# Kernel optimization log

Measured on AMD Instinct MI355X. Metric: run time of the kernel, lower is better.

The kernel has to match this reference:

```python
import jax, jax.numpy as jnp
import numpy as np

DIM = 768        # channel dim C
HEADS = 12       # num_heads
MAXLEN = 128     # max_seq_len == window length N
NW = 64          # num_windows
B = 4            # batch


def setup_inputs() -> dict:
    key = jax.random.key(0)
    k0, k1, k2, k3 = jax.random.split(key, 4)
    B_ = NW * B
    x = jax.random.normal(k0, (B_, MAXLEN, DIM), jnp.float32)
    mask = jnp.zeros((NW, MAXLEN, MAXLEN), jnp.float32)  # 0/-inf additive window mask
    qkv_w = jax.random.normal(k1, (3 * DIM, DIM), jnp.float32) * 0.02
    bias_table = jax.random.normal(k2, (2 * MAXLEN - 1, HEADS), jnp.float32) * 0.02
    proj_w = jax.random.normal(k3, (DIM, DIM), jnp.float32) * 0.02
    proj_b = jnp.zeros((DIM,), jnp.float32)
    return {"x": x, "mask": mask, "qkv_w": qkv_w, "bias_table": bias_table,
            "proj_w": proj_w, "proj_b": proj_b}


def reference(x, mask, qkv_w, bias_table, proj_w, proj_b):
    B_, N, C = x.shape
    H = HEADS
    hd = C // H
    scale = hd ** -0.5
    # qkv projection (no bias): (B_, N, 3, H, hd)
    qkv = (x @ qkv_w.T).reshape(B_, N, 3, H, hd)
    q = qkv[:, :, 0].transpose(0, 2, 1, 3) * scale  # (B_, H, N, hd)
    k = qkv[:, :, 1].transpose(0, 2, 1, 3)
    v = qkv[:, :, 2].transpose(0, 2, 1, 3)
    attn = jnp.einsum('bhnd,bhmd->bhnm', q, k)       # (B_, H, N, N)
    # relative position bias gather
    coords = jnp.arange(N)
    rel_idx = coords[:, None] - coords[None, :] + (MAXLEN - 1)  # (N, N)
    bias = bias_table[rel_idx]                        # (N, N, H)
    attn = attn + bias.transpose(2, 0, 1)[None]       # (B_, H, N, N)
    # window mask add (mask ndim == 3 branch)
    nW = mask.shape[0]
    attn = attn.reshape(B_ // nW, nW, H, N, N) + mask[None, :, None]
    attn = jax.nn.softmax(attn.reshape(B_, H, N, N), axis=-1)
    out = jnp.einsum('bhnm,bhmd->bhnd', attn, v)      # (B_, H, N, hd)
    out = out.transpose(0, 2, 1, 3).reshape(B_, N, C)
    return out @ proj_w.T + proj_b
```

## Files before the change

kernel.cpp:

```cpp
#include <hip/hip_runtime.h>
#include <hip/hip_bf16.h>
#include <stdint.h>

typedef unsigned short u16;
typedef __bf16 bf16x8 __attribute__((ext_vector_type(8)));
typedef float f32x4 __attribute__((ext_vector_type(4)));

__device__ __forceinline__ u16 f2bf(float f) {
  union { float f; uint32_t u; } v; v.f = f;
  uint32_t u = v.u;
  return (u16)((u + 0x7FFFu + ((u >> 16) & 1u)) >> 16);
}

__device__ __forceinline__ f32x4 mfma16(bf16x8 a, bf16x8 b, f32x4 c) {
  return __builtin_amdgcn_mfma_f32_16x16x32_bf16(a, b, c, 0, 0, 0);
}

#define GLOBAL_TO_LDS16(g, l)                                                  \
  __builtin_amdgcn_global_load_lds(                                            \
      (const __attribute__((address_space(1))) void*)(g),                      \
      (__attribute__((address_space(3))) void*)(l), 16, 0, 0)

__global__ void cvt_bf16_all(const float* __restrict__ x, u16* __restrict__ xb,
                             const float* __restrict__ qw, u16* __restrict__ qwb,
                             const float* __restrict__ pw, u16* __restrict__ pwb) {
  int blk = blockIdx.x;
  const float* src; u16* dst; int i;
  if (blk < 24576)        { src = x;  dst = xb;  i = blk * 256 + threadIdx.x; }
  else if (blk < 26304)   { src = qw; dst = qwb; i = (blk - 24576) * 256 + threadIdx.x; }
  else                    { src = pw; dst = pwb; i = (blk - 26304) * 256 + threadIdx.x; }
  float4 f = ((const float4*)src)[i];
  ushort4 o;
  o.x = f2bf(f.x); o.y = f2bf(f.y); o.z = f2bf(f.z); o.w = f2bf(f.w);
  ((ushort4*)dst)[i] = o;
}

template <bool SWAP>
__global__ __launch_bounds__(256) void qkv_gemm(
    const u16* __restrict__ A, const u16* __restrict__ Bt, int nbase,
    u16* __restrict__ q, u16* __restrict__ k, u16* __restrict__ vT) {
  const int K = 768;
  __shared__ u16 As[128 * 64];
  __shared__ u16 Bs[128 * 64];
  int tid = threadIdx.x;
  int wave = tid >> 6, lane = tid & 63;
  int quad = lane >> 4, lrow = lane & 15;
  int m0 = blockIdx.y * 128, n0 = nbase + blockIdx.x * 128;
  int wr = (wave >> 1) * 64, wc = (wave & 1) * 64;

  const u16* asrc[4]; const u16* bsrc[4]; int ldst[4];
#pragma unroll
  for (int s = 0; s < 4; s++) {
    int p = (wave * 4 + s) * 64 + lane;
    int row = p >> 3, cp = p & 7;
    int c = cp ^ (row & 7);
    asrc[s] = A + (size_t)(m0 + row) * K + c * 8;
    bsrc[s] = Bt + (size_t)(n0 + row) * K + c * 8;
    ldst[s] = p * 8;
  }
  f32x4 acc[4][4] = {};
  for (int k0 = 0; k0 < K; k0 += 64) {
#pragma unroll
    for (int s = 0; s < 4; s++) {
      GLOBAL_TO_LDS16(asrc[s] + k0, As + ldst[s]);
      GLOBAL_TO_LDS16(bsrc[s] + k0, Bs + ldst[s]);
    }
    __syncthreads();
#pragma unroll
    for (int kk = 0; kk < 2; kk++) {
      bf16x8 am[4], bn[4];
#pragma unroll
      for (int i = 0; i < 4; i++) {
        int r = wr + i * 16 + lrow;
        am[i] = *(const bf16x8*)(As + r * 64 + ((((kk << 2) | quad) ^ (r & 7)) << 3));
      }
#pragma unroll
      for (int j = 0; j < 4; j++) {
        int r = wc + j * 16 + lrow;
        bn[j] = *(const bf16x8*)(Bs + r * 64 + ((((kk << 2) | quad) ^ (r & 7)) << 3));
      }
#pragma unroll
      for (int i = 0; i < 4; i++)
#pragma unroll
        for (int j = 0; j < 4; j++)
          acc[i][j] = SWAP ? mfma16(bn[i], am[j], acc[i][j])
                           : mfma16(am[i], bn[j], acc[i][j]);
    }
    __syncthreads();
  }
  int b = m0 >> 7;
  if (SWAP) {
    int t = n0 / 768;
    float s = (t == 0) ? 0.125f : 1.0f;
    u16* dst = (t == 0) ? q : k;
#pragma unroll
    for (int i = 0; i < 4; i++) {
      int nb = (n0 - t * 768) + wc + i * 16 + quad * 4;
      int h = nb >> 6, d0 = nb & 63;
#pragma unroll
      for (int j = 0; j < 4; j++) {
        int seq = wr + j * 16 + lrow;
        ushort4 o;
        o.x = f2bf(acc[i][j][0] * s); o.y = f2bf(acc[i][j][1] * s);
        o.z = f2bf(acc[i][j][2] * s); o.w = f2bf(acc[i][j][3] * s);
        *(ushort4*)(dst + ((size_t)(b * 12 + h)) * 8192 + seq * 64 + d0) = o;
      }
    }
  } else {
#pragma unroll
    for (int j = 0; j < 4; j++) {
      int nb = (n0 - 1536) + wc + j * 16 + lrow;
      int h = nb >> 6, d = nb & 63;
#pragma unroll
      for (int i = 0; i < 4; i++) {
        int seq0 = wr + i * 16 + quad * 4;
        ushort4 o;
        o.x = f2bf(acc[i][j][0]); o.y = f2bf(acc[i][j][1]);
        o.z = f2bf(acc[i][j][2]); o.w = f2bf(acc[i][j][3]);
        *(ushort4*)(vT + ((size_t)(b * 12 + h)) * 8192 + d * 128 + seq0) = o;
      }
    }
  }
}

__global__ __launch_bounds__(512) void attn_kernel(
    const u16* __restrict__ q, const u16* __restrict__ k, const u16* __restrict__ vT,
    const float* __restrict__ mask, const float* __restrict__ bias_table,
    u16* __restrict__ attn_out) {
  __shared__ u16 smem[2 * 128 * 64];
  __shared__ u16 vTs[64 * 128];
  __shared__ float bias_s[255];
  u16* qs = smem;
  u16* ks = smem + 128 * 64;
  u16* ps = smem;
  int tid = threadIdx.x;
  int wave = tid >> 6, lane = tid & 63;
  int quad = lane >> 4, lrow = lane & 15;
  int bh = blockIdx.x;
  int b = bh / 12, h = bh - b * 12;
  int w = b & 63;
  if (tid < 255) bias_s[tid] = bias_table[tid * 12 + h];
  const u16* qg = q + (size_t)bh * 8192;
  const u16* kg = k + (size_t)bh * 8192;
  const u16* vg = vT + (size_t)bh * 8192;
#pragma unroll
  for (int s = 0; s < 2; s++) {
    int p = s * 512 + tid;
    int row = p >> 3, c = (p & 7) ^ (row & 7);
    GLOBAL_TO_LDS16(qg + row * 64 + c * 8, qs + p * 8);
    GLOBAL_TO_LDS16(kg + row * 64 + c * 8, ks + p * 8);
    int dd = p >> 4, cv = (p & 15) ^ (dd & 7);
    GLOBAL_TO_LDS16(vg + dd * 128 + cv * 8, vTs + p * 8);
  }
  __syncthreads();

  int row = wave * 16 + lrow;
  f32x4 sacc[8] = {};
#pragma unroll
  for (int kk = 0; kk < 2; kk++) {
    bf16x8 qf = *(const bf16x8*)(qs + row * 64 + ((((kk << 2) | quad) ^ (row & 7)) << 3));
#pragma unroll
    for (int i = 0; i < 8; i++) {
      int rk = i * 16 + lrow;
      bf16x8 kf = *(const bf16x8*)(ks + rk * 64 + ((((kk << 2) | quad) ^ (rk & 7)) << 3));
      sacc[i] = mfma16(kf, qf, sacc[i]);
    }
  }
  const float* mrow = mask + (size_t)w * 16384 + row * 128;
#pragma unroll
  for (int i = 0; i < 8; i++) {
    int c0 = i * 16 + quad * 4;
    float4 m4 = *(const float4*)(mrow + c0);
    sacc[i][0] += bias_s[row - (c0 + 0) + 127] + m4.x;
    sacc[i][1] += bias_s[row - (c0 + 1) + 127] + m4.y;
    sacc[i][2] += bias_s[row - (c0 + 2) + 127] + m4.z;
    sacc[i][3] += bias_s[row - (c0 + 3) + 127] + m4.w;
  }
  float mx = sacc[0][0];
#pragma unroll
  for (int i = 0; i < 8; i++)
#pragma unroll
    for (int r = 0; r < 4; r++) mx = fmaxf(mx, sacc[i][r]);
  mx = fmaxf(mx, __shfl_xor(mx, 16, 64));
  mx = fmaxf(mx, __shfl_xor(mx, 32, 64));
  float sum = 0.f;
#pragma unroll
  for (int i = 0; i < 8; i++)
#pragma unroll
    for (int r = 0; r < 4; r++) {
      float e = __expf(sacc[i][r] - mx);
      sacc[i][r] = e;
      sum += e;
    }
  sum += __shfl_xor(sum, 16, 64);
  sum += __shfl_xor(sum, 32, 64);
  float inv = 1.f / sum;
  __syncthreads();
#pragma unroll
  for (int i = 0; i < 8; i++) {
    int chunk = i * 2 + (quad >> 1);
    int pos = chunk ^ (row & 7);
    ushort4 o;
    o.x = f2bf(sacc[i][0] * inv); o.y = f2bf(sacc[i][1] * inv);
    o.z = f2bf(sacc[i][2] * inv); o.w = f2bf(sacc[i][3] * inv);
    *(ushort4*)(ps + row * 128 + pos * 8 + (quad & 1) * 4) = o;
  }
  __syncthreads();

  f32x4 oacc[4] = {};
#pragma unroll
  for (int kk = 0; kk < 4; kk++) {
    bf16x8 pf = *(const bf16x8*)(ps + row * 128 + ((((kk << 2) | quad) ^ (row & 7)) << 3));
#pragma unroll
    for (int jd = 0; jd < 4; jd++) {
      int rd = jd * 16 + lrow;
      bf16x8 vf = *(const bf16x8*)(vTs + rd * 128 + ((((kk << 2) | quad) ^ (rd & 7)) << 3));
      oacc[jd] = mfma16(vf, pf, oacc[jd]);
    }
  }
#pragma unroll
  for (int jd = 0; jd < 4; jd++) {
    int d0 = jd * 16 + quad * 4;
    int seq = wave * 16 + lrow;
    ushort4 o;
    o.x = f2bf(oacc[jd][0]); o.y = f2bf(oacc[jd][1]);
    o.z = f2bf(oacc[jd][2]); o.w = f2bf(oacc[jd][3]);
    *(ushort4*)(attn_out + ((size_t)(b * 128 + seq)) * 768 + h * 64 + d0) = o;
  }
}

__global__ __launch_bounds__(256) void proj_gemm(
    const u16* __restrict__ A, const u16* __restrict__ Bt,
    const float* __restrict__ bias, float* __restrict__ out) {
  const int K = 768;
  __shared__ u16 As[128 * 64];
  __shared__ u16 Bs[128 * 64];
  int tid = threadIdx.x;
  int wave = tid >> 6, lane = tid & 63;
  int quad = lane >> 4, lrow = lane & 15;
  int m0 = blockIdx.y * 128, n0 = blockIdx.x * 128;
  int wr = (wave >> 1) * 64, wc = (wave & 1) * 64;

  const u16* asrc[4]; const u16* bsrc[4]; int ldst[4];
#pragma unroll
  for (int s = 0; s < 4; s++) {
    int p = (wave * 4 + s) * 64 + lane;
    int row = p >> 3, c = (p & 7) ^ (row & 7);
    asrc[s] = A + (size_t)(m0 + row) * K + c * 8;
    bsrc[s] = Bt + (size_t)(n0 + row) * K + c * 8;
    ldst[s] = p * 8;
  }
  f32x4 acc[4][4] = {};
  for (int k0 = 0; k0 < K; k0 += 64) {
#pragma unroll
    for (int s = 0; s < 4; s++) {
      GLOBAL_TO_LDS16(asrc[s] + k0, As + ldst[s]);
      GLOBAL_TO_LDS16(bsrc[s] + k0, Bs + ldst[s]);
    }
    __syncthreads();
#pragma unroll
    for (int kk = 0; kk < 2; kk++) {
      bf16x8 am[4], bn[4];
#pragma unroll
      for (int i = 0; i < 4; i++) {
        int r = wr + i * 16 + lrow;
        am[i] = *(const bf16x8*)(As + r * 64 + ((((kk << 2) | quad) ^ (r & 7)) << 3));
      }
#pragma unroll
      for (int j = 0; j < 4; j++) {
        int r = wc + j * 16 + lrow;
        bn[j] = *(const bf16x8*)(Bs + r * 64 + ((((kk << 2) | quad) ^ (r & 7)) << 3));
      }
#pragma unroll
      for (int i = 0; i < 4; i++)
#pragma unroll
        for (int j = 0; j < 4; j++)
          acc[i][j] = mfma16(bn[i], am[j], acc[i][j]);
    }
    __syncthreads();
  }
#pragma unroll
  for (int i = 0; i < 4; i++) {
    int nb = n0 + wc + i * 16 + quad * 4;
    float4 b4 = *(const float4*)(bias + nb);
#pragma unroll
    for (int j = 0; j < 4; j++) {
      int m = m0 + wr + j * 16 + lrow;
      float4 o;
      o.x = acc[i][j][0] + b4.x; o.y = acc[i][j][1] + b4.y;
      o.z = acc[i][j][2] + b4.z; o.w = acc[i][j][3] + b4.w;
      *(float4*)(out + (size_t)m * 768 + nb) = o;
    }
  }
}

extern "C" void kernel_launch(void* const* d_in, const int* in_sizes, int n_in,
                              void* d_out, int out_size, void* d_ws, size_t ws_size,
                              hipStream_t stream) {
  const float* x          = (const float*)d_in[0];
  const float* mask       = (const float*)d_in[1];
  const float* qkv_w      = (const float*)d_in[2];
  const float* bias_table = (const float*)d_in[3];
  const float* proj_w     = (const float*)d_in[4];
  const float* proj_b     = (const float*)d_in[5];
  float* out = (float*)d_out;
  char* ws = (char*)d_ws;
  u16* q_b    = (u16*)(ws);
  u16* k_b    = (u16*)(ws + 50331648);
  u16* vT_b   = (u16*)(ws + 100663296);
  u16* x_b    = (u16*)(ws + 150994944);
  u16* qw_b   = (u16*)(ws + 201326592);
  u16* pw_b   = (u16*)(ws + 204865536);
  u16* attn_b = x_b;

  cvt_bf16_all<<<26880, 256, 0, stream>>>(x, x_b, qkv_w, qw_b, proj_w, pw_b);
  qkv_gemm<true><<<dim3(12, 256), 256, 0, stream>>>(x_b, qw_b, 0, q_b, k_b, vT_b);
  qkv_gemm<false><<<dim3(6, 256), 256, 0, stream>>>(x_b, qw_b, 1536, q_b, k_b, vT_b);
  attn_kernel<<<3072, 512, 0, stream>>>(q_b, k_b, vT_b, mask, bias_table, attn_b);
  proj_gemm<<<dim3(6, 256), 256, 0, stream>>>(attn_b, pw_b, proj_b, out);
}
```

Before: 481.5 us.

## Replace GEMM kernels with triple-buffered pipelined 512-thread GEMM with larger tiles

Unifies the QKV and projection GEMMs into one templated kernel that triple-buffers 32-wide K slices in LDS, issues async global-to-LDS loads two stages ahead, and waits on them with partial vmcnt counts instead of full __syncthreads. Tiles grow to 256x256 for Q/K (256x128 for V and proj) with 8 waves per block, a new XOR swizzle, and s_setprio around the MFMA bursts. The goal is to hide global load latency behind MFMA work and raise reuse per block. In exchange it uses more LDS and registers per block, and the hand-written waitcnt values must match the number of outstanding loads per stage.

```diff
diff --git a/kernel.cpp b/kernel.cpp
--- a/kernel.cpp
+++ b/kernel.cpp
@@ -20,6 +20,15 @@
   __builtin_amdgcn_global_load_lds(                                            \
       (const __attribute__((address_space(1))) void*)(g),                      \
       (__attribute__((address_space(3))) void*)(l), 16, 0, 0)
+
+template <int N>
+__device__ __forceinline__ void vm_wait_barrier() {
+  if constexpr (N == 0)      asm volatile("s_waitcnt vmcnt(0) lgkmcnt(0)" ::: "memory");
+  else if constexpr (N == 3) asm volatile("s_waitcnt vmcnt(3) lgkmcnt(0)" ::: "memory");
+  else                       asm volatile("s_waitcnt vmcnt(4) lgkmcnt(0)" ::: "memory");
+  __builtin_amdgcn_s_barrier();
+  asm volatile("" ::: "memory");
+}
 
 __global__ void cvt_bf16_all(const float* __restrict__ x, u16* __restrict__ xb,
                              const float* __restrict__ qw, u16* __restrict__ qwb,
@@ -35,89 +44,147 @@
   ((ushort4*)dst)[i] = o;
 }
 
-template <bool SWAP>
-__global__ __launch_bounds__(256) void qkv_gemm(
+template <int MODE>
+__global__ __launch_bounds__(512, (MODE == 0) ? 2 : 4) void gemm_pipe(
     const u16* __restrict__ A, const u16* __restrict__ Bt, int nbase,
-    u16* __restrict__ q, u16* __restrict__ k, u16* __restrict__ vT) {
+    u16* __restrict__ o_q, u16* __restrict__ o_k, u16* __restrict__ o_vT,
+    const float* __restrict__ bias, float* __restrict__ o_f32) {
+  constexpr int BN  = (MODE == 0) ? 256 : 128;
+  constexpr int WN  = (MODE == 0) ? 4 : 2;
+  constexpr int MF  = (MODE == 0) ? 8 : 4;
+  constexpr int NBS = (MODE == 0) ? 2 : 1;
+  constexpr int LPT = 2 + NBS;
+  constexpr int KT  = 24;
   const int K = 768;
-  __shared__ u16 As[128 * 64];
-  __shared__ u16 Bs[128 * 64];
+
+  __shared__ u16 As[3 * 256 * 32];
+  __shared__ u16 Bs[3 * BN * 32];
+
   int tid = threadIdx.x;
-  int wave = tid >> 6, lane = tid & 63;
+  int wid = tid >> 6, lane = tid & 63;
   int quad = lane >> 4, lrow = lane & 15;
-  int m0 = blockIdx.y * 128, n0 = nbase + blockIdx.x * 128;
-  int wr = (wave >> 1) * 64, wc = (wave & 1) * 64;
-
-  const u16* asrc[4]; const u16* bsrc[4]; int ldst[4];
-#pragma unroll
-  for (int s = 0; s < 4; s++) {
-    int p = (wave * 4 + s) * 64 + lane;
-    int row = p >> 3, cp = p & 7;
-    int c = cp ^ (row & 7);
-    asrc[s] = A + (size_t)(m0 + row) * K + c * 8;
-    bsrc[s] = Bt + (size_t)(n0 + row) * K + c * 8;
-    ldst[s] = p * 8;
-  }
-  f32x4 acc[4][4] = {};
-  for (int k0 = 0; k0 < K; k0 += 64) {
-#pragma unroll
-    for (int s = 0; s < 4; s++) {
-      GLOBAL_TO_LDS16(asrc[s] + k0, As + ldst[s]);
-      GLOBAL_TO_LDS16(bsrc[s] + k0, Bs + ldst[s]);
-    }
-    __syncthreads();
-#pragma unroll
-    for (int kk = 0; kk < 2; kk++) {
-      bf16x8 am[4], bn[4];
-#pragma unroll
-      for (int i = 0; i < 4; i++) {
-        int r = wr + i * 16 + lrow;
-        am[i] = *(const bf16x8*)(As + r * 64 + ((((kk << 2) | quad) ^ (r & 7)) << 3));
+  int wm = wid / WN, wn = wid % WN;
+  int m0 = blockIdx.y * 256;
+  int n0l = blockIdx.x * BN;
+  int n0g = nbase + n0l;
+
+  const u16* aSrc[2]; int aDst[2];
+#pragma unroll
+  for (int s = 0; s < 2; s++) {
+    int p = (wid + s * 8) * 64 + lane;
+    int r = p >> 2;
+    int c = (p & 3) ^ (r & 3) ^ ((r >> 2) & 3);
+    aSrc[s] = A + (size_t)(m0 + r) * K + c * 8;
+    aDst[s] = p * 8;
+  }
+  const u16* bSrc[NBS]; int bDst[NBS];
+#pragma unroll
+  for (int s = 0; s < NBS; s++) {
+    int p = (wid + s * 8) * 64 + lane;
+    int r = p >> 2;
+    int c = (p & 3) ^ (r & 3) ^ ((r >> 2) & 3);
+    bSrc[s] = Bt + (size_t)(n0g + r) * K + c * 8;
+    bDst[s] = p * 8;
+  }
+
+  f32x4 acc[MF][4] = {};
+
+  auto STAGE = [&](int koff, int slot) {
+#pragma unroll
+    for (int s = 0; s < 2; s++)
+      GLOBAL_TO_LDS16(aSrc[s] + koff, As + slot * 8192 + aDst[s]);
+#pragma unroll
+    for (int s = 0; s < NBS; s++)
+      GLOBAL_TO_LDS16(bSrc[s] + koff, Bs + slot * (BN * 32) + bDst[s]);
+  };
+
+  auto COMPUTE = [&](int slot) {
+    const u16* Ab = As + slot * 8192;
+    const u16* Bb = Bs + slot * (BN * 32);
+    bf16x8 af[MF], bfr[4];
+#pragma unroll
+    for (int m = 0; m < MF; m++) {
+      int r = wm * (MF * 16) + m * 16 + lrow;
+      af[m] = *(const bf16x8*)(Ab + r * 32 + ((quad ^ (r & 3) ^ ((r >> 2) & 3)) << 3));
+    }
+#pragma unroll
+    for (int n = 0; n < 4; n++) {
+      int r = wn * 64 + n * 16 + lrow;
+      bfr[n] = *(const bf16x8*)(Bb + r * 32 + ((quad ^ (r & 3) ^ ((r >> 2) & 3)) << 3));
+    }
+    __builtin_amdgcn_s_setprio(1);
+#pragma unroll
+    for (int m = 0; m < MF; m++)
+#pragma unroll
+      for (int n = 0; n < 4; n++)
+        acc[m][n] = (MODE != 1) ? mfma16(bfr[n], af[m], acc[m][n])
+                                : mfma16(af[m], bfr[n], acc[m][n]);
+    __builtin_amdgcn_s_setprio(0);
+  };
+
+  STAGE(0, 0);
+  STAGE(32, 1);
+  vm_wait_barrier<LPT>();
+
+  int cs = 0, ns = 2, koff = 64;
+  for (int t = 0; t < KT - 2; ++t) {
+    STAGE(koff, ns);
+    COMPUTE(cs);
+    vm_wait_barrier<LPT>();
+    koff += 32;
+    cs = (cs == 2) ? 0 : cs + 1;
+    ns = (ns == 2) ? 0 : ns + 1;
+  }
+  COMPUTE((KT - 2) % 3);
+  vm_wait_barrier<0>();
+  COMPUTE((KT - 1) % 3);
+
+  if constexpr (MODE == 0) {
+#pragma unroll
+    for (int n = 0; n < 4; n++) {
+      int nf = n0l + wn * 64 + n * 16 + quad * 4;
+      int t = nf >= 768;
+      int f = nf - (t ? 768 : 0);
+      u16* dst = t ? o_k : o_q;
+      float sc = t ? 1.0f : 0.125f;
+      int h = f >> 6, d0 = f & 63;
+#pragma unroll
+      for (int m = 0; m < MF; m++) {
+        int seqg = m0 + wm * 128 + m * 16 + lrow;
+        int b = seqg >> 7, s = seqg & 127;
+        ushort4 o;
+        o.x = f2bf(acc[m][n][0] * sc); o.y = f2bf(acc[m][n][1] * sc);
+        o.z = f2bf(acc[m][n][2] * sc); o.w = f2bf(acc[m][n][3] * sc);
+        *(ushort4*)(dst + ((size_t)(b * 12 + h)) * 8192 + s * 64 + d0) = o;
       }
-#pragma unroll
-      for (int j = 0; j < 4; j++) {
-        int r = wc + j * 16 + lrow;
-        bn[j] = *(const bf16x8*)(Bs + r * 64 + ((((kk << 2) | quad) ^ (r & 7)) << 3));
+    }
+  } else if constexpr (MODE == 1) {
+#pragma unroll
+    for (int n = 0; n < 4; n++) {
+      int f = n0l + wn * 64 + n * 16 + lrow;
+      int h = f >> 6, d = f & 63;
+#pragma unroll
+      for (int m = 0; m < MF; m++) {
+        int seq0 = m0 + wm * 64 + m * 16 + quad * 4;
+        int b = seq0 >> 7, s0 = seq0 & 127;
+        ushort4 o;
+        o.x = f2bf(acc[m][n][0]); o.y = f2bf(acc[m][n][1]);
+        o.z = f2bf(acc[m][n][2]); o.w = f2bf(acc[m][n][3]);
+        *(ushort4*)(o_vT + ((size_t)(b * 12 + h)) * 8192 + d * 128 + s0) = o;
       }
-#pragma unroll
-      for (int i = 0; i < 4; i++)
-#pragma unroll
-        for (int j = 0; j < 4; j++)
-          acc[i][j] = SWAP ? mfma16(bn[i], am[j], acc[i][j])
-                           : mfma16(am[i], bn[j], acc[i][j]);
-    }
-    __syncthreads();
-  }
-  int b = m0 >> 7;
-  if (SWAP) {
-    int t = n0 / 768;
-    float s = (t == 0) ? 0.125f : 1.0f;
-    u16* dst = (t == 0) ? q : k;
-#pragma unroll
-    for (int i = 0; i < 4; i++) {
-      int nb = (n0 - t * 768) + wc + i * 16 + quad * 4;
-      int h = nb >> 6, d0 = nb & 63;
-#pragma unroll
-      for (int j = 0; j < 4; j++) {
-        int seq = wr + j * 16 + lrow;
-        ushort4 o;
-        o.x = f2bf(acc[i][j][0] * s); o.y = f2bf(acc[i][j][1] * s);
-        o.z = f2bf(acc[i][j][2] * s); o.w = f2bf(acc[i][j][3] * s);
-        *(ushort4*)(dst + ((size_t)(b * 12 + h)) * 8192 + seq * 64 + d0) = o;
-      }
     }
   } else {
 #pragma unroll
-    for (int j = 0; j < 4; j++) {
-      int nb = (n0 - 1536) + wc + j * 16 + lrow;
-      int h = nb >> 6, d = nb & 63;
-#pragma unroll
-      for (int i = 0; i < 4; i++) {
-        int seq0 = wr + i * 16 + quad * 4;
-        ushort4 o;
-        o.x = f2bf(acc[i][j][0]); o.y = f2bf(acc[i][j][1]);
-        o.z = f2bf(acc[i][j][2]); o.w = f2bf(acc[i][j][3]);
-        *(ushort4*)(vT + ((size_t)(b * 12 + h)) * 8192 + d * 128 + seq0) = o;
+    for (int n = 0; n < 4; n++) {
+      int nf = n0l + wn * 64 + n * 16 + quad * 4;
+      float4 b4 = *(const float4*)(bias + nf);
+#pragma unroll
+      for (int m = 0; m < MF; m++) {
+        int mr = m0 + wm * 64 + m * 16 + lrow;
+        float4 o;
+        o.x = acc[m][n][0] + b4.x; o.y = acc[m][n][1] + b4.y;
+        o.z = acc[m][n][2] + b4.z; o.w = acc[m][n][3] + b4.w;
+        *(float4*)(o_f32 + (size_t)mr * 768 + nf) = o;
       }
     }
   }
@@ -229,71 +296,6 @@
   }
 }
 
-__global__ __launch_bounds__(256) void proj_gemm(
-    const u16* __restrict__ A, const u16* __restrict__ Bt,
-    const float* __restrict__ bias, float* __restrict__ out) {
-  const int K = 768;
-  __shared__ u16 As[128 * 64];
-  __shared__ u16 Bs[128 * 64];
-  int tid = threadIdx.x;
-  int wave = tid >> 6, lane = tid & 63;
-  int quad = lane >> 4, lrow = lane & 15;
-  int m0 = blockIdx.y * 128, n0 = blockIdx.x * 128;
-  int wr = (wave >> 1) * 64, wc = (wave & 1) * 64;
-
-  const u16* asrc[4]; const u16* bsrc[4]; int ldst[4];
-#pragma unroll
-  for (int s = 0; s < 4; s++) {
-    int p = (wave * 4 + s) * 64 + lane;
-    int row = p >> 3, c = (p & 7) ^ (row & 7);
-    asrc[s] = A + (size_t)(m0 + row) * K + c * 8;
-    bsrc[s] = Bt + (size_t)(n0 + row) * K + c * 8;
-    ldst[s] = p * 8;
-  }
-  f32x4 acc[4][4] = {};
-  for (int k0 = 0; k0 < K; k0 += 64) {
-#pragma unroll
-    for (int s = 0; s < 4; s++) {
-      GLOBAL_TO_LDS16(asrc[s] + k0, As + ldst[s]);
-      GLOBAL_TO_LDS16(bsrc[s] + k0, Bs + ldst[s]);
-    }
-    __syncthreads();
-#pragma unroll
-    for (int kk = 0; kk < 2; kk++) {
-      bf16x8 am[4], bn[4];
-#pragma unroll
-      for (int i = 0; i < 4; i++) {
-        int r = wr + i * 16 + lrow;
-        am[i] = *(const bf16x8*)(As + r * 64 + ((((kk << 2) | quad) ^ (r & 7)) << 3));
-      }
-#pragma unroll
-      for (int j = 0; j < 4; j++) {
-        int r = wc + j * 16 + lrow;
-        bn[j] = *(const bf16x8*)(Bs + r * 64 + ((((kk << 2) | quad) ^ (r & 7)) << 3));
-      }
-#pragma unroll
-      for (int i = 0; i < 4; i++)
-#pragma unroll
-        for (int j = 0; j < 4; j++)
-          acc[i][j] = mfma16(bn[i], am[j], acc[i][j]);
-    }
-    __syncthreads();
-  }
-#pragma unroll
-  for (int i = 0; i < 4; i++) {
-    int nb = n0 + wc + i * 16 + quad * 4;
-    float4 b4 = *(const float4*)(bias + nb);
-#pragma unroll
-    for (int j = 0; j < 4; j++) {
-      int m = m0 + wr + j * 16 + lrow;
-      float4 o;
-      o.x = acc[i][j][0] + b4.x; o.y = acc[i][j][1] + b4.y;
-      o.z = acc[i][j][2] + b4.z; o.w = acc[i][j][3] + b4.w;
-      *(float4*)(out + (size_t)m * 768 + nb) = o;
-    }
-  }
-}
-
 extern "C" void kernel_launch(void* const* d_in, const int* in_sizes, int n_in,
                               void* d_out, int out_size, void* d_ws, size_t ws_size,
                               hipStream_t stream) {
@@ -314,8 +316,11 @@
   u16* attn_b = x_b;
 
   cvt_bf16_all<<<26880, 256, 0, stream>>>(x, x_b, qkv_w, qw_b, proj_w, pw_b);
-  qkv_gemm<true><<<dim3(12, 256), 256, 0, stream>>>(x_b, qw_b, 0, q_b, k_b, vT_b);
-  qkv_gemm<false><<<dim3(6, 256), 256, 0, stream>>>(x_b, qw_b, 1536, q_b, k_b, vT_b);
+  gemm_pipe<0><<<dim3(6, 128), 512, 0, stream>>>(x_b, qw_b, 0,
+                                                 q_b, k_b, vT_b, nullptr, nullptr);
+  gemm_pipe<1><<<dim3(6, 128), 512, 0, stream>>>(x_b, qw_b, 1536,
+                                                 q_b, k_b, vT_b, nullptr, nullptr);
   attn_kernel<<<3072, 512, 0, stream>>>(q_b, k_b, vT_b, mask, bias_table, attn_b);
-  proj_gemm<<<dim3(6, 256), 256, 0, stream>>>(attn_b, pw_b, proj_b, out);
-}
+  gemm_pipe<2><<<dim3(6, 128), 512, 0, stream>>>(attn_b, pw_b, 0,
+                                                 nullptr, nullptr, nullptr, proj_b, out);
+}
```

Measured after the change: 510.2 us. 1.06x slower.
